# Optimization experiments

Hardware: AMD Instinct MI355X
Metric: run time of the kernel (lower is better)

Reference implementation:

```python
import jax, jax.numpy as jnp
import numpy as np

B, T, D, U = 32, 1024, 256, 256


def setup_inputs() -> dict:
    key = jax.random.key(0)
    k1, k2, k3 = jax.random.split(key, 3)
    x = jax.random.normal(k1, (B, T, D), dtype=jnp.float32)
    # glorot-normal-ish scale for weights
    kernel = jax.random.normal(k2, (D, 8 * U), dtype=jnp.float32) * np.sqrt(2.0 / (D + U)).astype(np.float32)
    recurrent_kernel = jax.random.normal(k3, (U, 8 * U), dtype=jnp.float32) * np.sqrt(2.0 / (U + U)).astype(np.float32)
    return {"x": x, "kernel": kernel, "recurrent_kernel": recurrent_kernel}


def _hard_sigmoid(v):
    # Keras hard_sigmoid: clip(0.2*x + 0.5, 0, 1)
    return jnp.clip(0.2 * v + 0.5, 0.0, 1.0)


def _lstm_dir(x, k4, rk4, units):
    # x: [B,T,D]; k4: [D,4U]; rk4: [U,4U]; gate order i, f, c, o (as in kernel slices)
    xg = jnp.einsum('btd,dg->tbg', x, k4)  # precompute input projections for all steps

    def step(carry, xg_t):
        h, c = carry
        g = xg_t + h @ rk4  # [B,4U] fused recurrent GEMM
        i = _hard_sigmoid(g[:, :units])
        f = _hard_sigmoid(g[:, units:2 * units])
        m = jnp.tanh(g[:, 2 * units:3 * units])
        o = _hard_sigmoid(g[:, 3 * units:])
        c_new = f * c + i * m
        h_new = o * jnp.tanh(c_new)
        return (h_new, c_new), h_new

    h0 = jnp.zeros((x.shape[0], units), x.dtype)
    _, hs = jax.lax.scan(step, (h0, h0), xg)  # hs: [T,B,U]
    return jnp.transpose(hs, (1, 0, 2))  # [B,T,U]


def reference(x, kernel, recurrent_kernel):
    units = recurrent_kernel.shape[0]
    # forward direction uses first 4*units columns
    out_f = _lstm_dir(x, kernel[:, :4 * units], recurrent_kernel[:, :4 * units], units)
    # backward direction: reverse time, run, reverse back
    out_b = _lstm_dir(x[:, ::-1], kernel[:, 4 * units:], recurrent_kernel[:, 4 * units:], units)[:, ::-1]
    return jnp.concatenate([out_f, out_b], axis=-1)  # [B,T,2U]
```

## Files before the change

### kernel.cpp

```cpp
#include <hip/hip_runtime.h>
#include <hip/hip_bf16.h>
#include <cstdint>

#define T_ 1024

typedef _Float16 f16;
typedef _Float16 f16x2 __attribute__((ext_vector_type(2)));
typedef _Float16 f16x4 __attribute__((ext_vector_type(4)));
typedef _Float16 f16x8 __attribute__((ext_vector_type(8)));
typedef float f32x4 __attribute__((ext_vector_type(4)));

static __device__ __forceinline__ f16x2 u2h(uint32_t u) {
    return __builtin_bit_cast(f16x2, u);
}

static __device__ __forceinline__ float hsig(float v) {
    return fminf(fmaxf(fmaf(v, 0.2f, 0.5f), 0.0f), 1.0f);
}

static __device__ __forceinline__ float tanh_f(float x) {
    float e = __expf(2.0f * x);
    return 1.0f - 2.0f / (e + 1.0f);
}

__global__ void convert_x(const float* __restrict__ x, f16* __restrict__ xh) {
    int i = blockIdx.x * blockDim.x + threadIdx.x;
    float4 v = ((const float4*)x)[i];
    f16x4 o;
    o[0] = (f16)v.x; o[1] = (f16)v.y; o[2] = (f16)v.z; o[3] = (f16)v.w;
    ((f16x4*)xh)[i] = o;
}

__global__ __launch_bounds__(256) void transpose_to_f16(const float* __restrict__ in,
                                                        f16* __restrict__ out) {
    __shared__ float tile[256][65];
    int g0 = blockIdx.x * 64;
    int tid = threadIdx.x;
#pragma unroll 4
    for (int it = 0; it < 64; ++it) {
        int idx = it * 256 + tid;
        int k = idx >> 6;
        int gi = idx & 63;
        tile[k][gi] = in[k * 2048 + g0 + gi];
    }
    __syncthreads();
#pragma unroll 4
    for (int it = 0; it < 64; ++it) {
        int idx = it * 256 + tid;
        int gi = idx >> 8;
        int k = idx & 255;
        out[(size_t)(g0 + gi) * 256 + k] = (f16)tile[k][gi];
    }
}

__global__ void zero_hx(unsigned long long* __restrict__ hx) {
    int i = blockIdx.x * blockDim.x + threadIdx.x;
    hx[i] = 0ull;
}

__global__ __launch_bounds__(256) void gemm_xk(const f16* __restrict__ A,
                                               const f16* __restrict__ Bt,
                                               f16* __restrict__ xg) {
    int nb = blockIdx.x;
    int mb = blockIdx.y;
    int tid = threadIdx.x;
    int l = tid & 63, w = tid >> 6;
    int wr = w >> 1, wc = w & 1;
    int row0 = mb * 128 + wr * 64;
    int col0 = nb * 128 + wc * 64;
    int lr = l & 15, lk = (l >> 4) * 8;

    f32x4 acc[4][4] = {};
    for (int k0 = 0; k0 < 256; k0 += 32) {
        f16x8 af[4], bf[4];
#pragma unroll
        for (int mi = 0; mi < 4; mi++)
            af[mi] = *(const f16x8*)&A[(row0 + mi * 16 + lr) * 256 + k0 + lk];
#pragma unroll
        for (int ni = 0; ni < 4; ni++)
            bf[ni] = *(const f16x8*)&Bt[(col0 + ni * 16 + lr) * 256 + k0 + lk];
#pragma unroll
        for (int mi = 0; mi < 4; mi++)
#pragma unroll
            for (int ni = 0; ni < 4; ni++)
                acc[mi][ni] = __builtin_amdgcn_mfma_f32_16x16x32_f16(af[mi], bf[ni], acc[mi][ni], 0, 0, 0);
    }
#pragma unroll
    for (int mi = 0; mi < 4; mi++) {
#pragma unroll
        for (int q = 0; q < 4; q++) {
            int row = row0 + mi * 16 + (l >> 4) * 4 + q;
            int b = row >> 10, t = row & 1023;
            long obase = (long)((t << 5) + b) * 2048;
#pragma unroll
            for (int ni = 0; ni < 4; ni++) {
                int col = col0 + ni * 16 + lr;
                xg[obase + col] = (f16)acc[mi][ni][q];
            }
        }
    }
}

#define FDOT(hu, wu) acc = __builtin_amdgcn_fdot2(u2h(hu), u2h(wu), acc, false)

__global__ __launch_bounds__(512, 2) void blstm_rec2(const f16* __restrict__ xg,
                                                     const uint32_t* __restrict__ wt,
                                                     unsigned long long* __restrict__ hx,
                                                     float* __restrict__ out) {
    __shared__ __align__(16) uint32_t h32[128];

    int bb = blockIdx.x;
    int p = bb & 63;
    int hf = bb >> 6;
    int d = p >> 5, b = p & 31;
    int j = threadIdx.x;
    int gate = j & 3, u = j >> 2;

    int col = (d << 10) + (gate << 8) + (hf << 7) + u;
    const uint32_t* wp = wt + (size_t)col * 128;
    const uint32_t* wpo = wp + (hf << 6);
    const uint32_t* wpp = wp + ((1 - hf) << 6);
    uint32_t w[128];
#pragma unroll
    for (int k = 0; k < 64; k++) w[k] = wpo[k];
#pragma unroll
    for (int k = 0; k < 64; k++) w[64 + k] = wpp[k];

    unsigned long long* mybuf = hx + (size_t)((p << 1) + hf) * 64;
    const unsigned long long* pbuf = hx + (size_t)((p << 1) + (1 - hf)) * 64;

    if (j < 128) h32[j] = 0u;

    float c = 0.0f;
    const f16* xgb = xg + (size_t)b * 2048 + col;
    int t0 = d ? (T_ - 1) : 0;
    float a = (float)xgb[(size_t)t0 << 11 << 5];
    __syncthreads();

    const uint4* hqo = ((const uint4*)h32) + (hf << 4);
    const uint4* hqp = ((const uint4*)h32) + ((1 - hf) << 4);

    for (int s = 0; s < T_; ++s) {
        int t = d ? (T_ - 1 - s) : s;
        float anext = 0.0f;
        if (s + 1 < T_) {
            int tn = d ? (T_ - 2 - s) : (s + 1);
            anext = (float)xgb[(size_t)tn << 16];
        }

        float acc = a;
#pragma unroll
        for (int q = 0; q < 16; q++) {
            uint4 hv = hqo[q];
            FDOT(hv.x, w[4 * q + 0]);
            FDOT(hv.y, w[4 * q + 1]);
            FDOT(hv.z, w[4 * q + 2]);
            FDOT(hv.w, w[4 * q + 3]);
        }
        if (s && j < 64) {
            unsigned long long v;
            do {
                v = __hip_atomic_load(&pbuf[j], __ATOMIC_RELAXED, __HIP_MEMORY_SCOPE_AGENT);
            } while ((uint32_t)(v >> 32) != (uint32_t)s);
            h32[((1 - hf) << 6) + j] = (uint32_t)v;
        }
        __syncthreads();
#pragma unroll
        for (int q = 0; q < 16; q++) {
            uint4 hv = hqp[q];
            FDOT(hv.x, w[64 + 4 * q + 0]);
            FDOT(hv.y, w[64 + 4 * q + 1]);
            FDOT(hv.z, w[64 + 4 * q + 2]);
            FDOT(hv.w, w[64 + 4 * q + 3]);
        }

        float g0 = acc;
        float g1 = __shfl_xor(g0, 1);
        float g2 = __shfl_xor(g0, 2);
        float g3 = __shfl_xor(g1, 2);
        bool b0 = gate & 1, b1 = gate & 2;
        float lo = b0 ? g1 : g0, hi = b0 ? g3 : g2;
        float lo2 = b0 ? g0 : g1, hi2 = b0 ? g2 : g3;
        float gi = b1 ? hi : lo, gf = b1 ? hi2 : lo2;
        float gm = b1 ? lo : hi, go = b1 ? lo2 : hi2;

        float iv = hsig(gi), fv = hsig(gf), mv = tanh_f(gm), ov = hsig(go);
        c = fv * c + iv * mv;
        float h = ov * tanh_f(c);

        if (gate == 0)
            out[(size_t)((b << 10) + t) * 512 + (d << 8) + (hf << 7) + u] = h;

        uint32_t hb = (uint32_t)__builtin_bit_cast(uint16_t, (f16)h);
        uint32_t ob = __shfl_xor(hb, 4);
        if ((j & 7) == 0) {
            uint32_t word = hb | (ob << 16);
            h32[(hf << 6) + (j >> 3)] = word;
            __hip_atomic_store(&mybuf[j >> 3],
                               ((unsigned long long)(uint32_t)(s + 1) << 32) | (unsigned long long)word,
                               __ATOMIC_RELAXED, __HIP_MEMORY_SCOPE_AGENT);
        }
        a = anext;
        __syncthreads();
    }
}

extern "C" void kernel_launch(void* const* d_in, const int* in_sizes, int n_in,
                              void* d_out, int out_size, void* d_ws, size_t ws_size,
                              hipStream_t stream) {
    const float* x = (const float*)d_in[0];
    const float* kern = (const float*)d_in[1];
    const float* rk = (const float*)d_in[2];
    float* out = (float*)d_out;

    uint8_t* ws = (uint8_t*)d_ws;
    f16* xh = (f16*)ws;
    f16* kh_t = (f16*)(ws + (size_t)16 * 1024 * 1024);
    uint32_t* wt = (uint32_t*)(ws + (size_t)17 * 1024 * 1024);
    f16* xgh = (f16*)(ws + (size_t)18 * 1024 * 1024);
    unsigned long long* hx = (unsigned long long*)(ws + (size_t)146 * 1024 * 1024);

    convert_x<<<8192, 256, 0, stream>>>(x, xh);
    transpose_to_f16<<<32, 256, 0, stream>>>(kern, kh_t);
    transpose_to_f16<<<32, 256, 0, stream>>>(rk, (f16*)wt);
    gemm_xk<<<dim3(16, 256), 256, 0, stream>>>(xh, kh_t, xgh);
    zero_hx<<<16, 512, 0, stream>>>(hx);
    blstm_rec2<<<128, 512, 0, stream>>>(xgh, wt, hx, out);
}
```

Before: 1.767 ms.

## Split recurrent LSTM across four blocks per sequence with double-buffered exchange

Each (direction,batch) recurrence now runs on four cooperating blocks instead of two, with each block owning 64 hidden units. Threads split the K dimension in halves and combine results by a shuffle, so each thread holds 64 weight words instead of 128. The hidden-state exchange uses parity double-buffered global slots and reads from three peers. The aim is more CUs working on the serial recurrence and less per-step dot-product latency, at the cost of more cross-block synchronization traffic per step.

```diff
diff --git a/kernel.cpp b/kernel.cpp
--- a/kernel.cpp
+++ b/kernel.cpp
@@ -9,6 +9,7 @@
 typedef _Float16 f16x4 __attribute__((ext_vector_type(4)));
 typedef _Float16 f16x8 __attribute__((ext_vector_type(8)));
 typedef float f32x4 __attribute__((ext_vector_type(4)));
+typedef uint32_t u32x16 __attribute__((ext_vector_type(16)));
 
 static __device__ __forceinline__ f16x2 u2h(uint32_t u) {
     return __builtin_bit_cast(f16x2, u);
@@ -101,44 +102,45 @@
     }
 }
 
-#define FDOT(hu, wu) acc = __builtin_amdgcn_fdot2(u2h(hu), u2h(wu), acc, false)
-
-__global__ __launch_bounds__(512, 2) void blstm_rec2(const f16* __restrict__ xg,
+#define FDOT(hu, wu, acc) acc = __builtin_amdgcn_fdot2(u2h(hu), u2h(wu), acc, false)
+
+#define DOT4(hv, W, E, acc)                \
+    FDOT(hv.x, (W)[(E) + 0], acc);         \
+    FDOT(hv.y, (W)[(E) + 1], acc);         \
+    FDOT(hv.z, (W)[(E) + 2], acc);         \
+    FDOT(hv.w, (W)[(E) + 3], acc);
+
+__global__ __launch_bounds__(512, 2) void blstm_rec4(const f16* __restrict__ xg,
                                                      const uint32_t* __restrict__ wt,
                                                      unsigned long long* __restrict__ hx,
                                                      float* __restrict__ out) {
     __shared__ __align__(16) uint32_t h32[128];
 
     int bb = blockIdx.x;
-    int p = bb & 63;
-    int hf = bb >> 6;
+    int qu = (bb >> 3) & 3;
+    int p = ((bb & 7) << 3) + (bb >> 5);
     int d = p >> 5, b = p & 31;
     int j = threadIdx.x;
-    int gate = j & 3, u = j >> 2;
-
-    int col = (d << 10) + (gate << 8) + (hf << 7) + u;
-    const uint32_t* wp = wt + (size_t)col * 128;
-    const uint32_t* wpo = wp + (hf << 6);
-    const uint32_t* wpp = wp + ((1 - hf) << 6);
-    uint32_t w[128];
-#pragma unroll
-    for (int k = 0; k < 64; k++) w[k] = wpo[k];
-#pragma unroll
-    for (int k = 0; k < 64; k++) w[64 + k] = wpp[k];
-
-    unsigned long long* mybuf = hx + (size_t)((p << 1) + hf) * 64;
-    const unsigned long long* pbuf = hx + (size_t)((p << 1) + (1 - hf)) * 64;
+    int gate = j & 3;
+    int kh = (j >> 2) & 1;
+    int uu = ((j >> 3) & 7) + ((j >> 6) << 3);
+
+    int col = (d << 10) + (gate << 8) + (qu << 6) + uu;
+    const u32x16* wp = (const u32x16*)(wt + (size_t)col * 128 + (kh << 6));
+    u32x16 A0 = wp[0], A1 = wp[1], A2 = wp[2], A3 = wp[3];
+
+    unsigned long long* pub0 = hx + (size_t)((p << 2) + qu) * 32;
+    unsigned long long* pub1 = pub0 + 256 * 32;
 
     if (j < 128) h32[j] = 0u;
 
     float c = 0.0f;
     const f16* xgb = xg + (size_t)b * 2048 + col;
     int t0 = d ? (T_ - 1) : 0;
-    float a = (float)xgb[(size_t)t0 << 11 << 5];
+    float a = (float)xgb[(size_t)t0 << 16];
     __syncthreads();
 
-    const uint4* hqo = ((const uint4*)h32) + (hf << 4);
-    const uint4* hqp = ((const uint4*)h32) + ((1 - hf) << 4);
+    const uint4* hq = ((const uint4*)h32) + (kh << 4);
 
     for (int s = 0; s < T_; ++s) {
         int t = d ? (T_ - 1 - s) : s;
@@ -148,31 +150,43 @@
             anext = (float)xgb[(size_t)tn << 16];
         }
 
-        float acc = a;
-#pragma unroll
-        for (int q = 0; q < 16; q++) {
-            uint4 hv = hqo[q];
-            FDOT(hv.x, w[4 * q + 0]);
-            FDOT(hv.y, w[4 * q + 1]);
-            FDOT(hv.z, w[4 * q + 2]);
-            FDOT(hv.w, w[4 * q + 3]);
-        }
-        if (s && j < 64) {
+        if (s && j < 96) {
+            int rq = (qu + 1 + (j >> 5)) & 3;
+            int w = j & 31;
+            const unsigned long long* rb =
+                hx + (size_t)(((s & 1) << 8) + (p << 2) + rq) * 32;
             unsigned long long v;
             do {
-                v = __hip_atomic_load(&pbuf[j], __ATOMIC_RELAXED, __HIP_MEMORY_SCOPE_AGENT);
+                v = __hip_atomic_load(&rb[w], __ATOMIC_RELAXED, __HIP_MEMORY_SCOPE_AGENT);
             } while ((uint32_t)(v >> 32) != (uint32_t)s);
-            h32[((1 - hf) << 6) + j] = (uint32_t)v;
+            h32[(rq << 5) + w] = (uint32_t)v;
         }
         __syncthreads();
-#pragma unroll
-        for (int q = 0; q < 16; q++) {
-            uint4 hv = hqp[q];
-            FDOT(hv.x, w[64 + 4 * q + 0]);
-            FDOT(hv.y, w[64 + 4 * q + 1]);
-            FDOT(hv.z, w[64 + 4 * q + 2]);
-            FDOT(hv.w, w[64 + 4 * q + 3]);
-        }
+
+        float accA = kh ? 0.0f : a;
+        float accB = 0.0f;
+        {
+            uint4 h0 = hq[0], h1 = hq[1], h2 = hq[2], h3 = hq[3];
+            DOT4(h0, A0, 0, accA) DOT4(h1, A0, 4, accB)
+            DOT4(h2, A0, 8, accA) DOT4(h3, A0, 12, accB)
+        }
+        {
+            uint4 h0 = hq[4], h1 = hq[5], h2 = hq[6], h3 = hq[7];
+            DOT4(h0, A1, 0, accA) DOT4(h1, A1, 4, accB)
+            DOT4(h2, A1, 8, accA) DOT4(h3, A1, 12, accB)
+        }
+        {
+            uint4 h0 = hq[8], h1 = hq[9], h2 = hq[10], h3 = hq[11];
+            DOT4(h0, A2, 0, accA) DOT4(h1, A2, 4, accB)
+            DOT4(h2, A2, 8, accA) DOT4(h3, A2, 12, accB)
+        }
+        {
+            uint4 h0 = hq[12], h1 = hq[13], h2 = hq[14], h3 = hq[15];
+            DOT4(h0, A3, 0, accA) DOT4(h1, A3, 4, accB)
+            DOT4(h2, A3, 8, accA) DOT4(h3, A3, 12, accB)
+        }
+        float acc = accA + accB;
+        acc += __shfl_xor(acc, 4);
 
         float g0 = acc;
         float g1 = __shfl_xor(g0, 1);
@@ -188,15 +202,17 @@
         c = fv * c + iv * mv;
         float h = ov * tanh_f(c);
 
-        if (gate == 0)
-            out[(size_t)((b << 10) + t) * 512 + (d << 8) + (hf << 7) + u] = h;
+        if ((j & 7) == 0)
+            out[(size_t)((b << 10) + t) * 512 + (d << 8) + (qu << 6) + uu] = h;
 
         uint32_t hb = (uint32_t)__builtin_bit_cast(uint16_t, (f16)h);
-        uint32_t ob = __shfl_xor(hb, 4);
-        if ((j & 7) == 0) {
+        uint32_t ob = __shfl_xor(hb, 8);
+        if ((j & 15) == 0) {
             uint32_t word = hb | (ob << 16);
-            h32[(hf << 6) + (j >> 3)] = word;
-            __hip_atomic_store(&mybuf[j >> 3],
+            int kp = uu >> 1;
+            h32[(qu << 5) + kp] = word;
+            unsigned long long* pub = ((s + 1) & 1) ? pub1 : pub0;
+            __hip_atomic_store(&pub[kp],
                                ((unsigned long long)(uint32_t)(s + 1) << 32) | (unsigned long long)word,
                                __ATOMIC_RELAXED, __HIP_MEMORY_SCOPE_AGENT);
         }
@@ -224,6 +240,6 @@
     transpose_to_f16<<<32, 256, 0, stream>>>(kern, kh_t);
     transpose_to_f16<<<32, 256, 0, stream>>>(rk, (f16*)wt);
     gemm_xk<<<dim3(16, 256), 256, 0, stream>>>(xh, kh_t, xgh);
-    zero_hx<<<16, 512, 0, stream>>>(hx);
-    blstm_rec2<<<128, 512, 0, stream>>>(xgh, wt, hx, out);
-}
+    zero_hx<<<32, 512, 0, stream>>>(hx);
+    blstm_rec4<<<256, 512, 0, stream>>>(xgh, wt, hx, out);
+}
```

Result: no change. 1.740 ms (-1.5%).
